# Kernel tuning notes

Measured on AMD Instinct MI355X. Metric: run time of the kernel, lower is better.

The kernel has to match this reference:

```python
import jax, jax.numpy as jnp
import numpy as np

NUM_GRAPHS = 64
NODE_SZ = 200
FEAT = 200
HID = 256          # hidden_size; each signed branch outputs HID//2
HALF = HID // 2
N_NODES = NUM_GRAPHS * NODE_SZ
N_EDGES = 409600
NUM_LAYERS = 3


def _lin_init(key, out_f, in_f):
    kw, kb = jax.random.split(key)
    s = 1.0 / np.sqrt(in_f)
    W = jax.random.uniform(kw, (out_f, in_f), minval=-s, maxval=s, dtype=jnp.float32)
    b = jax.random.uniform(kb, (out_f,), minval=-s, maxval=s, dtype=jnp.float32)
    return W, b


def setup_inputs() -> dict:
    key = jax.random.key(0)
    ks = jax.random.split(key, 16)
    x = jax.random.normal(ks[0], (N_NODES, FEAT), dtype=jnp.float32)
    edge_index = jax.random.randint(ks[1], (2, N_EDGES), 0, N_NODES, dtype=jnp.int64)
    edge_weight = jax.random.normal(ks[2], (N_EDGES,), dtype=jnp.float32)
    batch = jnp.repeat(jnp.arange(NUM_GRAPHS, dtype=jnp.int64), NODE_SZ)

    # signed conv layer params: layer0 in=FEAT, layers 1..: in=HID; each lin maps 2*in -> HALF
    Wp0, bp0 = _lin_init(ks[3], HALF, 2 * FEAT)
    Wn0, bn0 = _lin_init(ks[4], HALF, 2 * FEAT)
    Wp1, bp1 = _lin_init(ks[5], HALF, 2 * HID)
    Wn1, bn1 = _lin_init(ks[6], HALF, 2 * HID)
    Wp2, bp2 = _lin_init(ks[7], HALF, 2 * HID)
    Wn2, bn2 = _lin_init(ks[8], HALF, 2 * HID)
    Wr, br = _lin_init(ks[9], HID, NODE_SZ * HID)   # readout_lin
    Wl, bl = _lin_init(ks[10], 1, HID)              # final lin
    return dict(x=x, edge_index=edge_index, edge_weight=edge_weight, batch=batch,
                Wp0=Wp0, bp0=bp0, Wn0=Wn0, bn0=bn0,
                Wp1=Wp1, bp1=bp1, Wn1=Wn1, bn1=bn1,
                Wp2=Wp2, bp2=bp2, Wn2=Wn2, bn2=bn2,
                Wr=Wr, br=br, Wl=Wl, bl=bl)


def _signed_conv(x, src, dst, w, Wp, bp, Wn, bn):
    # edge-weighted signed mean aggregation, split by weight sign
    xs = x[src]                                   # [E, D] gather
    pw = jnp.where(w > 0, w, 0.0)
    nw = jnp.where(w < 0, -w, 0.0)
    agg_p = jax.ops.segment_sum(pw[:, None] * xs, dst, num_segments=N_NODES)
    agg_n = jax.ops.segment_sum(nw[:, None] * xs, dst, num_segments=N_NODES)
    deg_p = jax.ops.segment_sum((w > 0).astype(x.dtype), dst, num_segments=N_NODES)
    deg_n = jax.ops.segment_sum((w < 0).astype(x.dtype), dst, num_segments=N_NODES)
    agg_p = agg_p / jnp.maximum(deg_p, 1.0)[:, None]
    agg_n = agg_n / jnp.maximum(deg_n, 1.0)[:, None]
    hp = jnp.concatenate([agg_p, x], -1) @ Wp.T + bp
    hn = jnp.concatenate([agg_n, x], -1) @ Wn.T + bn
    return jnp.concatenate([hp, hn], -1)          # [N, HID]


def reference(x, edge_index, edge_weight, batch,
              Wp0, bp0, Wn0, bn0, Wp1, bp1, Wn1, bn1, Wp2, bp2, Wn2, bn2,
              Wr, br, Wl, bl):
    src, dst = edge_index[0], edge_index[1]
    convs = [(Wp0, bp0, Wn0, bn0), (Wp1, bp1, Wn1, bn1), (Wp2, bp2, Wn2, bn2)]
    h = x
    for i, (Wp, bp, Wn, bn) in enumerate(convs):
        h = _signed_conv(h, src, dst, edge_weight, Wp, bp, Wn, bn)
        if i < NUM_LAYERS - 1:
            h = jax.nn.leaky_relu(h, negative_slope=0.01)
    # per-graph readout: batch is contiguous with NODE_SZ nodes per graph,
    # so the boolean-mask+view loop is exactly a reshape.
    g = h.reshape(NUM_GRAPHS, NODE_SZ * HID)
    g = g @ Wr.T + br                             # [G, HID]
    # dropout(p=0.5) is identity in eval mode
    return g @ Wl.T + bl                          # [G, 1]
```

## Files before the change

### kernel.cpp

```cpp
#include <hip/hip_runtime.h>

#define NUM_GRAPHS 64
#define NODE_SZ    200
#define FEAT       200
#define HID        256
#define HALF       128
#define N_NODES    (NUM_GRAPHS * NODE_SZ)
#define KREAD      (NODE_SZ * HID)
#define KSTRIDE    512
#define HBLK       128

typedef unsigned short ushort_t;
typedef unsigned int uint_t;
typedef __attribute__((ext_vector_type(8))) short bf16x8;
typedef __attribute__((ext_vector_type(4))) float f32x4;

#define GAS(p) ((const __attribute__((address_space(1))) void*)(p))
#define LAS(p) ((__attribute__((address_space(3))) void*)(p))

__device__ __forceinline__ float bf2f(ushort_t u) {
    union { unsigned int i; float f; } v; v.i = ((unsigned int)u) << 16; return v.f;
}
__device__ __forceinline__ ushort_t f2bf(float f) {
    union { float f; unsigned int i; } v; v.f = f;
    unsigned int x = v.i;
    unsigned int r = (x + 0x7fffu + ((x >> 16) & 1u)) >> 16;
    return (ushort_t)r;
}

__global__ __launch_bounds__(1024) void bhist_kernel(const int* __restrict__ ei,
                                                     const float* __restrict__ ew,
                                                     uint_t* __restrict__ bh, int E) {
    __shared__ uint_t h[N_NODES];
    for (int i = threadIdx.x; i < N_NODES; i += 1024) h[i] = 0;
    __syncthreads();
    int b = blockIdx.x;
    int epb = (E + HBLK - 1) / HBLK;
    int e0 = b * epb, e1 = min(e0 + epb, E);
    for (int e = e0 + threadIdx.x; e < e1; e += 1024) {
        int dst = ei[E + e];
        float w = ew[e];
        if (w > 0.0f)      atomicAdd(&h[dst], 1u);
        else if (w < 0.0f) atomicAdd(&h[dst], 0x10000u);
    }
    __syncthreads();
    uint_t* out = bh + (size_t)b * N_NODES;
    for (int i = threadIdx.x * 4; i < N_NODES; i += 4096)
        *(uint4*)&out[i] = *(const uint4*)&h[i];
}

__global__ void colpref_kernel(uint_t* __restrict__ bh, int* __restrict__ counts,
                               int* __restrict__ cnt_p) {
    int n = blockIdx.x * 256 + threadIdx.x;
    if (n >= N_NODES) return;
    uint_t seq = 0;
#pragma unroll 1
    for (int b = 0; b < HBLK; b += 8) {
        uint_t v[8];
#pragma unroll
        for (int j = 0; j < 8; ++j) v[j] = bh[(size_t)(b + j) * N_NODES + n];
#pragma unroll
        for (int j = 0; j < 8; ++j) {
            bh[(size_t)(b + j) * N_NODES + n] = seq;
            seq += v[j];
        }
    }
    counts[n] = (int)((seq & 0xffffu) + (seq >> 16));
    cnt_p[n]  = (int)(seq & 0xffffu);
}

__global__ __launch_bounds__(1024) void scan_kernel(const int* __restrict__ counts,
                                                    const int* __restrict__ cnt_p,
                                                    uint2* __restrict__ obnd, int n) {
    const int PER = 13;
    int t = threadIdx.x;
    int start = t * PER;
    int local[PER];
    int sum = 0;
#pragma unroll
    for (int i = 0; i < PER; ++i) {
        int idx = start + i;
        int v = (idx < n) ? counts[idx] : 0;
        local[i] = sum;
        sum += v;
    }
    int lane = t & 63, wid = t >> 6;
    int inc = sum;
#pragma unroll
    for (int d = 1; d < 64; d <<= 1) {
        int up = __shfl_up(inc, d);
        if (lane >= d) inc += up;
    }
    __shared__ int wsum[16], woff[16];
    if (lane == 63) wsum[wid] = inc;
    __syncthreads();
    if (t < 16) {
        int acc = 0;
        for (int j = 0; j < 16; ++j) if (j < t) acc += wsum[j];
        woff[t] = acc;
    }
    __syncthreads();
    int base = woff[wid] + (inc - sum);
#pragma unroll
    for (int i = 0; i < PER; ++i) {
        int idx = start + i;
        if (idx < n) {
            uint_t off = (uint_t)(base + local[i]);
            obnd[idx] = make_uint2(off, off + (uint_t)cnt_p[idx]);
        }
    }
    if (t == 1023) {
        uint_t tot = (uint_t)(base + sum);
        obnd[n] = make_uint2(tot, tot);
    }
}

__global__ __launch_bounds__(1024) void scat_prep_kernel(
        const int* __restrict__ ei, const float* __restrict__ ew,
        const uint_t* __restrict__ bh, const uint2* __restrict__ obnd,
        uint2* __restrict__ es, int E,
        const float* __restrict__ W0p, const float* __restrict__ W0n,
        const float* __restrict__ W1p, const float* __restrict__ W1n,
        const float* __restrict__ W2p, const float* __restrict__ W2n,
        const float* __restrict__ x,
        ushort_t* __restrict__ wcast, ushort_t* __restrict__ xb) {
    __shared__ uint_t cur[N_NODES];
    int bx = blockIdx.x;
    if (bx < HBLK) {
        const uint_t* pref = bh + (size_t)bx * N_NODES;
        for (int i = threadIdx.x * 4; i < N_NODES; i += 4096)
            *(uint4*)&cur[i] = *(const uint4*)&pref[i];
        __syncthreads();
        int epb = (E + HBLK - 1) / HBLK;
        int e0 = bx * epb, e1 = min(e0 + epb, E);
        for (int e = e0 + threadIdx.x; e < e1; e += 1024) {
            int src = ei[e];
            int dst = ei[E + e];
            float w = ew[e];
            if (w > 0.0f) {
                uint_t old = atomicAdd(&cur[dst], 1u);
                uint_t pos = obnd[dst].x + (old & 0xffffu);
                es[pos] = make_uint2((uint_t)src, __float_as_uint(w));
            } else if (w < 0.0f) {
                uint_t old = atomicAdd(&cur[dst], 0x10000u);
                uint_t pos = obnd[dst].y + (old >> 16);
                es[pos] = make_uint2((uint_t)src, __float_as_uint(-w));
            }
        }
    } else if (bx < 512) {
        int idx = (bx - 128) * 1024 + threadIdx.x;
        int task = idx >> 16;
        int within = idx & 65535;
        const float* W = (task == 0) ? W0p : (task == 1) ? W0n : (task == 2) ? W1p
                       : (task == 3) ? W1n : (task == 4) ? W2p : W2n;
        int K2 = (task < 2) ? 400 : 512;
        int row = within >> 9;
        int col = within & (KSTRIDE - 1);
        wcast[task * 65536 + within] = (col < K2) ? f2bf(W[(size_t)row * K2 + col]) : (ushort_t)0;
    } else {
        int i = ((bx - 512) * 1024 + threadIdx.x) * 4;
        if (i < N_NODES * FEAT) {
            float4 v = *(const float4*)&x[i];
            ushort4 o;
            o.x = f2bf(v.x); o.y = f2bf(v.y); o.z = f2bf(v.z); o.w = f2bf(v.w);
            *(ushort4*)&xb[i] = o;
        }
    }
}

template <int D>
__global__ __launch_bounds__(256) void agg_kernel(
        const ushort_t* __restrict__ hb,
        const uint2* __restrict__ obnd,
        const uint2* __restrict__ es,
        ushort_t* __restrict__ Ap, ushort_t* __restrict__ An) {
    constexpr int ACT = D / 4;
    int lane = threadIdx.x & 63;
    int wv   = threadIdx.x >> 6;
    int n = blockIdx.x * 4 + wv;
    int c0 = min(lane, ACT - 1) * 4;
    uint2 ob = obnd[n];
    uint_t off = ob.x, mid = ob.y, end = obnd[n + 1].x;

    float ap[4] = {0.f, 0.f, 0.f, 0.f};
    float an[4] = {0.f, 0.f, 0.f, 0.f};

#pragma unroll 1
    for (int phase = 0; phase < 2; ++phase) {
        uint_t lo = phase ? mid : off;
        uint_t hi = phase ? end : mid;
        float* acc = phase ? an : ap;
#pragma unroll 1
        for (uint_t base = lo; base < hi; base += 64) {
            int cnt = (int)min(64u, hi - base);
            uint2 rec = es[base + (uint_t)min(lane, cnt - 1)];
            int i = 0;
#pragma unroll 1
            for (; i + 8 <= cnt; i += 8) {
                int s[8]; float w[8]; uint2 p[8];
#pragma unroll
                for (int j = 0; j < 8; ++j) {
                    s[j] = __shfl((int)rec.x, i + j);
                    w[j] = __uint_as_float((uint_t)__shfl((int)rec.y, i + j));
                }
#pragma unroll
                for (int j = 0; j < 8; ++j) p[j] = *(const uint2*)&hb[(size_t)s[j] * D + c0];
#pragma unroll
                for (int j = 0; j < 8; ++j) {
                    const ushort_t* q = (const ushort_t*)&p[j];
#pragma unroll
                    for (int c = 0; c < 4; ++c) acc[c] = fmaf(w[j], bf2f(q[c]), acc[c]);
                }
            }
#pragma unroll 1
            for (; i < cnt; ++i) {
                int s = __shfl((int)rec.x, i);
                float w = __uint_as_float((uint_t)__shfl((int)rec.y, i));
                uint2 pk = *(const uint2*)&hb[(size_t)s * D + c0];
                const ushort_t* q = (const ushort_t*)&pk;
#pragma unroll
                for (int c = 0; c < 4; ++c) acc[c] = fmaf(w, bf2f(q[c]), acc[c]);
            }
        }
    }

    size_t rb = (size_t)n * KSTRIDE;
    if (lane < ACT) {
        float dp = fmaxf((float)(mid - off), 1.0f);
        float dn = fmaxf((float)(end - mid), 1.0f);
        uint2 pk = *(const uint2*)&hb[(size_t)n * D + c0];
        const ushort_t* p = (const ushort_t*)&pk;
        ushort4 os = {p[0], p[1], p[2], p[3]};
        ushort4 op, on;
        op.x = f2bf(ap[0] / dp); op.y = f2bf(ap[1] / dp);
        op.z = f2bf(ap[2] / dp); op.w = f2bf(ap[3] / dp);
        on.x = f2bf(an[0] / dn); on.y = f2bf(an[1] / dn);
        on.z = f2bf(an[2] / dn); on.w = f2bf(an[3] / dn);
        *(ushort4*)&Ap[rb + c0] = op;
        *(ushort4*)&An[rb + c0] = on;
        *(ushort4*)&Ap[rb + D + c0] = os;
        *(ushort4*)&An[rb + D + c0] = os;
    }
    if (D == 200 && lane >= 50 && lane < 54) {
        ushort4 z = {0, 0, 0, 0};
        *(ushort4*)&Ap[rb + 400 + (lane - 50) * 4] = z;
        *(ushort4*)&An[rb + 400 + (lane - 50) * 4] = z;
    }
}

template <int KSTEPS, bool LEAKY>
__global__ __launch_bounds__(256) void conv_mfma(
        const ushort_t* __restrict__ Ap, const ushort_t* __restrict__ An,
        const ushort_t* __restrict__ Wpb, const ushort_t* __restrict__ Wnb,
        const float* __restrict__ bp, const float* __restrict__ bn,
        ushort_t* __restrict__ hout) {
    __shared__ __align__(16) ushort_t As[2][32 * 32];
    __shared__ __align__(16) ushort_t Bs[2][128 * 32];
    int mBase = blockIdx.x * 32;
    bool neg = (blockIdx.y != 0);
    const ushort_t* A    = neg ? An : Ap;
    const ushort_t* W    = neg ? Wnb : Wpb;
    const float*    bias = neg ? bn : bp;
    int tid  = threadIdx.x;
    int lane = tid & 63;
    int wv   = tid >> 6;
    int r    = lane & 15;
    int quad = lane >> 4;

    int rowA = tid >> 2, colA = (tid & 3) * 8;
    const ushort_t* gA  = A + (size_t)(mBase + (rowA & 31)) * KSTRIDE + colA;
    const ushort_t* gB0 = W + (size_t)rowA * KSTRIDE + colA;
    const ushort_t* gB1 = W + (size_t)(rowA + 64) * KSTRIDE + colA;

    f32x4 acc00 = {0.f,0.f,0.f,0.f}, acc01 = {0.f,0.f,0.f,0.f};
    f32x4 acc10 = {0.f,0.f,0.f,0.f}, acc11 = {0.f,0.f,0.f,0.f};

    if (tid < 128)
        __builtin_amdgcn_global_load_lds(GAS(gA), LAS(&As[0][wv * 512]), 16, 0, 0);
    __builtin_amdgcn_global_load_lds(GAS(gB0), LAS(&Bs[0][wv * 512]), 16, 0, 0);
    __builtin_amdgcn_global_load_lds(GAS(gB1), LAS(&Bs[0][2048 + wv * 512]), 16, 0, 0);

    for (int kt = 0; kt < KSTEPS; ++kt) {
        int cur = kt & 1;
        __syncthreads();
        if (kt + 1 < KSTEPS) {
            int kB = (kt + 1) * 32;
            if (tid < 128)
                __builtin_amdgcn_global_load_lds(GAS(gA + kB), LAS(&As[cur ^ 1][wv * 512]), 16, 0, 0);
            __builtin_amdgcn_global_load_lds(GAS(gB0 + kB), LAS(&Bs[cur ^ 1][wv * 512]), 16, 0, 0);
            __builtin_amdgcn_global_load_lds(GAS(gB1 + kB), LAS(&Bs[cur ^ 1][2048 + wv * 512]), 16, 0, 0);
        }
        bf16x8 a0 = *(const bf16x8*)&As[cur][r * 32 + quad * 8];
        bf16x8 a1 = *(const bf16x8*)&As[cur][(16 + r) * 32 + quad * 8];
        bf16x8 b0 = *(const bf16x8*)&Bs[cur][(wv * 32 + r) * 32 + quad * 8];
        bf16x8 b1 = *(const bf16x8*)&Bs[cur][(wv * 32 + 16 + r) * 32 + quad * 8];
        acc00 = __builtin_amdgcn_mfma_f32_16x16x32_bf16(a0, b0, acc00, 0, 0, 0);
        acc01 = __builtin_amdgcn_mfma_f32_16x16x32_bf16(a0, b1, acc01, 0, 0, 0);
        acc10 = __builtin_amdgcn_mfma_f32_16x16x32_bf16(a1, b0, acc10, 0, 0, 0);
        acc11 = __builtin_amdgcn_mfma_f32_16x16x32_bf16(a1, b1, acc11, 0, 0, 0);
    }
    int colOff = neg ? HALF : 0;
#pragma unroll
    for (int jn = 0; jn < 2; ++jn) {
        int cl = wv * 32 + jn * 16 + r;
        float bv = bias[cl];
        f32x4 am0 = jn ? acc01 : acc00;
        f32x4 am1 = jn ? acc11 : acc10;
#pragma unroll
        for (int reg = 0; reg < 4; ++reg) {
            int m0 = mBase + quad * 4 + reg;
            int m1 = m0 + 16;
            float v0 = am0[reg] + bv;
            float v1 = am1[reg] + bv;
            if (LEAKY) {
                v0 = (v0 > 0.0f) ? v0 : 0.01f * v0;
                v1 = (v1 > 0.0f) ? v1 : 0.01f * v1;
            }
            hout[(size_t)m0 * HID + colOff + cl] = f2bf(v0);
            hout[(size_t)m1 * HID + colOff + cl] = f2bf(v1);
        }
    }
}

__global__ __launch_bounds__(256) void readout_mfma(
        const ushort_t* __restrict__ h, const float* __restrict__ Wr,
        float* __restrict__ partial) {
    __shared__ __align__(16) ushort_t As[64 * 32];
    __shared__ __align__(16) ushort_t Bs[64 * 32];
    int nBase  = blockIdx.x * 64;
    int kStart = blockIdx.y * 800;
    int tid  = threadIdx.x;
    int lane = tid & 63;
    int wv   = tid >> 6;
    int r    = lane & 15;
    int quad = lane >> 4;

    f32x4 acc[4];
#pragma unroll
    for (int j = 0; j < 4; ++j) acc[j] = (f32x4){0.f, 0.f, 0.f, 0.f};

    for (int kt = 0; kt < 25; ++kt) {
        int kBase = kStart + kt * 32;
        int lin = tid * 8;
        int row = lin >> 5, col = lin & 31;
        *(uint4*)&As[lin] = *(const uint4*)&h[(size_t)row * KREAD + kBase + col];
        {
            const float* wp = &Wr[(size_t)(nBase + row) * KREAD + kBase + col];
            float4 f0 = *(const float4*)&wp[0];
            float4 f1 = *(const float4*)&wp[4];
            ushort4 b0, b1;
            b0.x = f2bf(f0.x); b0.y = f2bf(f0.y); b0.z = f2bf(f0.z); b0.w = f2bf(f0.w);
            b1.x = f2bf(f1.x); b1.y = f2bf(f1.y); b1.z = f2bf(f1.z); b1.w = f2bf(f1.w);
            *(ushort4*)&Bs[lin]     = b0;
            *(ushort4*)&Bs[lin + 4] = b1;
        }
        __syncthreads();
        bf16x8 a = *(const bf16x8*)&As[(wv * 16 + r) * 32 + quad * 8];
#pragma unroll
        for (int j = 0; j < 4; ++j) {
            bf16x8 b = *(const bf16x8*)&Bs[(j * 16 + r) * 32 + quad * 8];
            acc[j] = __builtin_amdgcn_mfma_f32_16x16x32_bf16(a, b, acc[j], 0, 0, 0);
        }
        __syncthreads();
    }
    float* out = partial + (size_t)blockIdx.y * (64 * HID);
#pragma unroll
    for (int j = 0; j < 4; ++j) {
        int c = nBase + j * 16 + r;
#pragma unroll
        for (int reg = 0; reg < 4; ++reg) {
            int g = wv * 16 + quad * 4 + reg;
            out[g * HID + c] = acc[j][reg];
        }
    }
}

__global__ void final_kernel(const float* __restrict__ partial, const float* __restrict__ br,
                             const float* __restrict__ Wl, const float* __restrict__ bl,
                             float* __restrict__ out) {
    int g = blockIdx.x;
    int c = threadIdx.x;
    float s = 0.0f;
#pragma unroll 4
    for (int k = 0; k < 64; ++k) s += partial[(size_t)k * (64 * HID) + g * HID + c];
    float v = (s + br[c]) * Wl[c];
#pragma unroll
    for (int d = 32; d > 0; d >>= 1) v += __shfl_down(v, d);
    __shared__ float sh[4];
    if ((c & 63) == 0) sh[c >> 6] = v;
    __syncthreads();
    if (c == 0) out[g] = sh[0] + sh[1] + sh[2] + sh[3] + bl[0];
}

extern "C" void kernel_launch(void* const* d_in, const int* in_sizes, int n_in,
                              void* d_out, int out_size, void* d_ws, size_t ws_size,
                              hipStream_t stream) {
    const float* x  = (const float*)d_in[0];
    const int*   ei = (const int*)d_in[1];
    const float* ew = (const float*)d_in[2];
    const float* Wp0 = (const float*)d_in[4];
    const float* bp0 = (const float*)d_in[5];
    const float* Wn0 = (const float*)d_in[6];
    const float* bn0 = (const float*)d_in[7];
    const float* Wp1 = (const float*)d_in[8];
    const float* bp1 = (const float*)d_in[9];
    const float* Wn1 = (const float*)d_in[10];
    const float* bn1 = (const float*)d_in[11];
    const float* Wp2 = (const float*)d_in[12];
    const float* bp2 = (const float*)d_in[13];
    const float* Wn2 = (const float*)d_in[14];
    const float* bn2 = (const float*)d_in[15];
    const float* Wr  = (const float*)d_in[16];
    const float* br  = (const float*)d_in[17];
    const float* Wl  = (const float*)d_in[18];
    const float* bl  = (const float*)d_in[19];
    const int E = in_sizes[1] / 2;

    char* ws = (char*)d_ws;
    float*    partial = (float*)(ws + 0);
    uint_t*   bh      = (uint_t*)(ws + 4194304);
    int*      counts  = (int*)(ws + 10747904);
    int*      cnt_p   = (int*)(ws + 10799104);
    uint2*    obnd    = (uint2*)(ws + 10850304);
    uint2*    es      = (uint2*)(ws + 10952768);
    ushort_t* Ap      = (ushort_t*)(ws + 14229568);
    ushort_t* An      = (ushort_t*)(ws + 27336768);
    ushort_t* hA      = (ushort_t*)(ws + 40443968);
    ushort_t* hB      = (ushort_t*)(ws + 46997568);
    ushort_t* wcast   = (ushort_t*)(ws + 53551168);
    ushort_t* xb      = (ushort_t*)(ws + 54337600);

    ushort_t* w0p = wcast + 0 * 65536;
    ushort_t* w0n = wcast + 1 * 65536;
    ushort_t* w1p = wcast + 2 * 65536;
    ushort_t* w1n = wcast + 3 * 65536;
    ushort_t* w2p = wcast + 4 * 65536;
    ushort_t* w2n = wcast + 5 * 65536;

    hipLaunchKernelGGL(bhist_kernel, dim3(HBLK), dim3(1024), 0, stream, ei, ew, bh, E);
    hipLaunchKernelGGL(colpref_kernel, dim3((N_NODES + 255) / 256), dim3(256), 0, stream,
                       bh, counts, cnt_p);
    hipLaunchKernelGGL(scan_kernel, dim3(1), dim3(1024), 0, stream, counts, cnt_p, obnd, N_NODES);
    hipLaunchKernelGGL(scat_prep_kernel, dim3(1137), dim3(1024), 0, stream,
                       ei, ew, bh, obnd, es, E,
                       Wp0, Wn0, Wp1, Wn1, Wp2, Wn2, x, wcast, xb);

    hipLaunchKernelGGL((agg_kernel<FEAT>), dim3(N_NODES / 4), dim3(256), 0, stream,
                       xb, obnd, es, Ap, An);
    hipLaunchKernelGGL((conv_mfma<13, true>), dim3(N_NODES / 32, 2), dim3(256), 0, stream,
                       Ap, An, w0p, w0n, bp0, bn0, hA);
    hipLaunchKernelGGL((agg_kernel<HID>), dim3(N_NODES / 4), dim3(256), 0, stream,
                       hA, obnd, es, Ap, An);
    hipLaunchKernelGGL((conv_mfma<16, true>), dim3(N_NODES / 32, 2), dim3(256), 0, stream,
                       Ap, An, w1p, w1n, bp1, bn1, hB);
    hipLaunchKernelGGL((agg_kernel<HID>), dim3(N_NODES / 4), dim3(256), 0, stream,
                       hB, obnd, es, Ap, An);
    hipLaunchKernelGGL((conv_mfma<16, false>), dim3(N_NODES / 32, 2), dim3(256), 0, stream,
                       Ap, An, w2p, w2n, bp2, bn2, hA);

    hipLaunchKernelGGL(readout_mfma, dim3(4, 64), dim3(256), 0, stream, hA, Wr, partial);
    hipLaunchKernelGGL(final_kernel, dim3(NUM_GRAPHS), dim3(256), 0, stream,
                       partial, br, Wl, bl, (float*)d_out);
}
```

Baseline: 310.4 us.

## Transform node features before aggregation instead of aggregating then transforming

Reorders each signed conv layer by linearity: a single GEMM first projects each node's features through the concatenated weight blocks (W_agg_p, W_agg_n, W_self_p, W_self_n) into a 512-wide Y. A combine kernel then gathers only the 128-wide projected rows per edge, scales by the inverse degree and adds the self term, bias and LeakyReLU. The gather moves 128 bf16 values per edge instead of 200 or 256, and the wide concatenated Ap/An buffers disappear. In exchange the GEMM output is twice as wide, and the aggregation now sums bf16-rounded projections, which changes rounding.

```diff
diff --git a/kernel.cpp b/kernel.cpp
--- a/kernel.cpp
+++ b/kernel.cpp
@@ -7,7 +7,6 @@
 #define HALF       128
 #define N_NODES    (NUM_GRAPHS * NODE_SZ)
 #define KREAD      (NODE_SZ * HID)
-#define KSTRIDE    512
 #define HBLK       128
 
 typedef unsigned short ushort_t;
@@ -123,7 +122,7 @@
         const float* __restrict__ W1p, const float* __restrict__ W1n,
         const float* __restrict__ W2p, const float* __restrict__ W2n,
         const float* __restrict__ x,
-        ushort_t* __restrict__ wcast, ushort_t* __restrict__ xb) {
+        ushort_t* __restrict__ wall, ushort_t* __restrict__ xb) {
     __shared__ uint_t cur[N_NODES];
     int bx = blockIdx.x;
     if (bx < HBLK) {
@@ -149,118 +148,41 @@
         }
     } else if (bx < 512) {
         int idx = (bx - 128) * 1024 + threadIdx.x;
-        int task = idx >> 16;
-        int within = idx & 65535;
-        const float* W = (task == 0) ? W0p : (task == 1) ? W0n : (task == 2) ? W1p
-                       : (task == 3) ? W1n : (task == 4) ? W2p : W2n;
-        int K2 = (task < 2) ? 400 : 512;
-        int row = within >> 9;
-        int col = within & (KSTRIDE - 1);
-        wcast[task * 65536 + within] = (col < K2) ? f2bf(W[(size_t)row * K2 + col]) : (ushort_t)0;
+        int layer = idx >> 17;
+        int within = idx & 131071;
+        int rr = within >> 8;
+        int col = within & 255;
+        const float* Wp = (layer == 0) ? W0p : (layer == 1) ? W1p : W2p;
+        const float* Wn = (layer == 0) ? W0n : (layer == 1) ? W1n : W2n;
+        int Ks = (layer == 0) ? 200 : 256;
+        int q = rr >> 7;
+        const float* Wsrc = (q & 1) ? Wn : Wp;
+        int row = rr & 127;
+        int scol = col + ((q >> 1) ? Ks : 0);
+        float v = (col < Ks) ? Wsrc[(size_t)row * (2 * Ks) + scol] : 0.0f;
+        wall[idx] = f2bf(v);
     } else {
-        int i = ((bx - 512) * 1024 + threadIdx.x) * 4;
-        if (i < N_NODES * FEAT) {
-            float4 v = *(const float4*)&x[i];
-            ushort4 o;
+        int idx = (bx - 512) * 1024 + threadIdx.x;
+        int n = idx >> 6;
+        int c0 = (idx & 63) * 4;
+        ushort4 o = {0, 0, 0, 0};
+        if (c0 < 200) {
+            float4 v = *(const float4*)&x[(size_t)n * 200 + c0];
             o.x = f2bf(v.x); o.y = f2bf(v.y); o.z = f2bf(v.z); o.w = f2bf(v.w);
-            *(ushort4*)&xb[i] = o;
-        }
-    }
-}
-
-template <int D>
-__global__ __launch_bounds__(256) void agg_kernel(
-        const ushort_t* __restrict__ hb,
-        const uint2* __restrict__ obnd,
-        const uint2* __restrict__ es,
-        ushort_t* __restrict__ Ap, ushort_t* __restrict__ An) {
-    constexpr int ACT = D / 4;
-    int lane = threadIdx.x & 63;
-    int wv   = threadIdx.x >> 6;
-    int n = blockIdx.x * 4 + wv;
-    int c0 = min(lane, ACT - 1) * 4;
-    uint2 ob = obnd[n];
-    uint_t off = ob.x, mid = ob.y, end = obnd[n + 1].x;
-
-    float ap[4] = {0.f, 0.f, 0.f, 0.f};
-    float an[4] = {0.f, 0.f, 0.f, 0.f};
-
-#pragma unroll 1
-    for (int phase = 0; phase < 2; ++phase) {
-        uint_t lo = phase ? mid : off;
-        uint_t hi = phase ? end : mid;
-        float* acc = phase ? an : ap;
-#pragma unroll 1
-        for (uint_t base = lo; base < hi; base += 64) {
-            int cnt = (int)min(64u, hi - base);
-            uint2 rec = es[base + (uint_t)min(lane, cnt - 1)];
-            int i = 0;
-#pragma unroll 1
-            for (; i + 8 <= cnt; i += 8) {
-                int s[8]; float w[8]; uint2 p[8];
-#pragma unroll
-                for (int j = 0; j < 8; ++j) {
-                    s[j] = __shfl((int)rec.x, i + j);
-                    w[j] = __uint_as_float((uint_t)__shfl((int)rec.y, i + j));
-                }
-#pragma unroll
-                for (int j = 0; j < 8; ++j) p[j] = *(const uint2*)&hb[(size_t)s[j] * D + c0];
-#pragma unroll
-                for (int j = 0; j < 8; ++j) {
-                    const ushort_t* q = (const ushort_t*)&p[j];
-#pragma unroll
-                    for (int c = 0; c < 4; ++c) acc[c] = fmaf(w[j], bf2f(q[c]), acc[c]);
-                }
-            }
-#pragma unroll 1
-            for (; i < cnt; ++i) {
-                int s = __shfl((int)rec.x, i);
-                float w = __uint_as_float((uint_t)__shfl((int)rec.y, i));
-                uint2 pk = *(const uint2*)&hb[(size_t)s * D + c0];
-                const ushort_t* q = (const ushort_t*)&pk;
-#pragma unroll
-                for (int c = 0; c < 4; ++c) acc[c] = fmaf(w, bf2f(q[c]), acc[c]);
-            }
-        }
-    }
-
-    size_t rb = (size_t)n * KSTRIDE;
-    if (lane < ACT) {
-        float dp = fmaxf((float)(mid - off), 1.0f);
-        float dn = fmaxf((float)(end - mid), 1.0f);
-        uint2 pk = *(const uint2*)&hb[(size_t)n * D + c0];
-        const ushort_t* p = (const ushort_t*)&pk;
-        ushort4 os = {p[0], p[1], p[2], p[3]};
-        ushort4 op, on;
-        op.x = f2bf(ap[0] / dp); op.y = f2bf(ap[1] / dp);
-        op.z = f2bf(ap[2] / dp); op.w = f2bf(ap[3] / dp);
-        on.x = f2bf(an[0] / dn); on.y = f2bf(an[1] / dn);
-        on.z = f2bf(an[2] / dn); on.w = f2bf(an[3] / dn);
-        *(ushort4*)&Ap[rb + c0] = op;
-        *(ushort4*)&An[rb + c0] = on;
-        *(ushort4*)&Ap[rb + D + c0] = os;
-        *(ushort4*)&An[rb + D + c0] = os;
-    }
-    if (D == 200 && lane >= 50 && lane < 54) {
-        ushort4 z = {0, 0, 0, 0};
-        *(ushort4*)&Ap[rb + 400 + (lane - 50) * 4] = z;
-        *(ushort4*)&An[rb + 400 + (lane - 50) * 4] = z;
-    }
-}
-
-template <int KSTEPS, bool LEAKY>
-__global__ __launch_bounds__(256) void conv_mfma(
-        const ushort_t* __restrict__ Ap, const ushort_t* __restrict__ An,
-        const ushort_t* __restrict__ Wpb, const ushort_t* __restrict__ Wnb,
-        const float* __restrict__ bp, const float* __restrict__ bn,
-        ushort_t* __restrict__ hout) {
+        }
+        *(ushort4*)&xb[(size_t)n * 256 + c0] = o;
+    }
+}
+
+template <int KSTEPS>
+__global__ __launch_bounds__(256) void gemm_mfma(
+        const ushort_t* __restrict__ A,
+        const ushort_t* __restrict__ B,
+        ushort_t* __restrict__ Y) {
     __shared__ __align__(16) ushort_t As[2][32 * 32];
     __shared__ __align__(16) ushort_t Bs[2][128 * 32];
     int mBase = blockIdx.x * 32;
-    bool neg = (blockIdx.y != 0);
-    const ushort_t* A    = neg ? An : Ap;
-    const ushort_t* W    = neg ? Wnb : Wpb;
-    const float*    bias = neg ? bn : bp;
+    int nBase = blockIdx.y * 128;
     int tid  = threadIdx.x;
     int lane = tid & 63;
     int wv   = tid >> 6;
@@ -268,9 +190,9 @@
     int quad = lane >> 4;
 
     int rowA = tid >> 2, colA = (tid & 3) * 8;
-    const ushort_t* gA  = A + (size_t)(mBase + (rowA & 31)) * KSTRIDE + colA;
-    const ushort_t* gB0 = W + (size_t)rowA * KSTRIDE + colA;
-    const ushort_t* gB1 = W + (size_t)(rowA + 64) * KSTRIDE + colA;
+    const ushort_t* gA  = A + (size_t)(mBase + (rowA & 31)) * 256 + colA;
+    const ushort_t* gB0 = B + (size_t)(nBase + rowA) * 256 + colA;
+    const ushort_t* gB1 = B + (size_t)(nBase + rowA + 64) * 256 + colA;
 
     f32x4 acc00 = {0.f,0.f,0.f,0.f}, acc01 = {0.f,0.f,0.f,0.f};
     f32x4 acc10 = {0.f,0.f,0.f,0.f}, acc11 = {0.f,0.f,0.f,0.f};
@@ -299,27 +221,94 @@
         acc10 = __builtin_amdgcn_mfma_f32_16x16x32_bf16(a1, b0, acc10, 0, 0, 0);
         acc11 = __builtin_amdgcn_mfma_f32_16x16x32_bf16(a1, b1, acc11, 0, 0, 0);
     }
-    int colOff = neg ? HALF : 0;
 #pragma unroll
     for (int jn = 0; jn < 2; ++jn) {
-        int cl = wv * 32 + jn * 16 + r;
-        float bv = bias[cl];
+        int cl = nBase + wv * 32 + jn * 16 + r;
         f32x4 am0 = jn ? acc01 : acc00;
         f32x4 am1 = jn ? acc11 : acc10;
 #pragma unroll
         for (int reg = 0; reg < 4; ++reg) {
             int m0 = mBase + quad * 4 + reg;
-            int m1 = m0 + 16;
-            float v0 = am0[reg] + bv;
-            float v1 = am1[reg] + bv;
-            if (LEAKY) {
-                v0 = (v0 > 0.0f) ? v0 : 0.01f * v0;
-                v1 = (v1 > 0.0f) ? v1 : 0.01f * v1;
+            Y[(size_t)m0 * 512 + cl]        = f2bf(am0[reg]);
+            Y[(size_t)(m0 + 16) * 512 + cl] = f2bf(am1[reg]);
+        }
+    }
+}
+
+template <bool LEAKY>
+__global__ __launch_bounds__(256) void aggcomb_kernel(
+        const ushort_t* __restrict__ Y,
+        const uint2* __restrict__ obnd,
+        const uint2* __restrict__ es,
+        const float* __restrict__ bp, const float* __restrict__ bn,
+        ushort_t* __restrict__ out) {
+    int lane = threadIdx.x & 63;
+    int wv   = threadIdx.x >> 6;
+    int n = blockIdx.x * 4 + wv;
+    int c0 = lane * 2;
+    uint2 ob = obnd[n];
+    uint_t off = ob.x, mid = ob.y, end = obnd[n + 1].x;
+
+    float accp[2] = {0.f, 0.f};
+    float accn[2] = {0.f, 0.f};
+
+#pragma unroll 1
+    for (int phase = 0; phase < 2; ++phase) {
+        uint_t lo = phase ? mid : off;
+        uint_t hi = phase ? end : mid;
+        float* acc = phase ? accn : accp;
+        const ushort_t* Yb = Y + (phase ? 128 : 0) + c0;
+#pragma unroll 1
+        for (uint_t base = lo; base < hi; base += 64) {
+            int cnt = (int)min(64u, hi - base);
+            uint2 rec = es[base + (uint_t)min(lane, cnt - 1)];
+            int i = 0;
+#pragma unroll 1
+            for (; i + 8 <= cnt; i += 8) {
+                int s[8]; float w[8]; uint_t u[8];
+#pragma unroll
+                for (int j = 0; j < 8; ++j) {
+                    s[j] = __shfl((int)rec.x, i + j);
+                    w[j] = __uint_as_float((uint_t)__shfl((int)rec.y, i + j));
+                }
+#pragma unroll
+                for (int j = 0; j < 8; ++j) u[j] = *(const uint_t*)&Yb[(size_t)s[j] * 512];
+#pragma unroll
+                for (int j = 0; j < 8; ++j) {
+                    acc[0] = fmaf(w[j], bf2f((ushort_t)(u[j] & 0xffffu)), acc[0]);
+                    acc[1] = fmaf(w[j], bf2f((ushort_t)(u[j] >> 16)), acc[1]);
+                }
             }
-            hout[(size_t)m0 * HID + colOff + cl] = f2bf(v0);
-            hout[(size_t)m1 * HID + colOff + cl] = f2bf(v1);
-        }
-    }
+#pragma unroll 1
+            for (; i < cnt; ++i) {
+                int s = __shfl((int)rec.x, i);
+                float w = __uint_as_float((uint_t)__shfl((int)rec.y, i));
+                uint_t u = *(const uint_t*)&Yb[(size_t)s * 512];
+                acc[0] = fmaf(w, bf2f((ushort_t)(u & 0xffffu)), acc[0]);
+                acc[1] = fmaf(w, bf2f((ushort_t)(u >> 16)), acc[1]);
+            }
+        }
+    }
+
+    float dp = fmaxf((float)(mid - off), 1.0f);
+    float dn = fmaxf((float)(end - mid), 1.0f);
+    float rp = 1.0f / dp, rn = 1.0f / dn;
+    uint_t zp = *(const uint_t*)&Y[(size_t)n * 512 + 256 + c0];
+    uint_t zn = *(const uint_t*)&Y[(size_t)n * 512 + 384 + c0];
+    float vp0 = fmaf(accp[0], rp, bf2f((ushort_t)(zp & 0xffffu)) + bp[c0]);
+    float vp1 = fmaf(accp[1], rp, bf2f((ushort_t)(zp >> 16))     + bp[c0 + 1]);
+    float vn0 = fmaf(accn[0], rn, bf2f((ushort_t)(zn & 0xffffu)) + bn[c0]);
+    float vn1 = fmaf(accn[1], rn, bf2f((ushort_t)(zn >> 16))     + bn[c0 + 1]);
+    if (LEAKY) {
+        vp0 = (vp0 > 0.0f) ? vp0 : 0.01f * vp0;
+        vp1 = (vp1 > 0.0f) ? vp1 : 0.01f * vp1;
+        vn0 = (vn0 > 0.0f) ? vn0 : 0.01f * vn0;
+        vn1 = (vn1 > 0.0f) ? vn1 : 0.01f * vn1;
+    }
+    uint_t op = (uint_t)f2bf(vp0) | ((uint_t)f2bf(vp1) << 16);
+    uint_t on = (uint_t)f2bf(vn0) | ((uint_t)f2bf(vn1) << 16);
+    *(uint_t*)&out[(size_t)n * 256 + c0]       = op;
+    *(uint_t*)&out[(size_t)n * 256 + 128 + c0] = on;
 }
 
 __global__ __launch_bounds__(256) void readout_mfma(
@@ -423,40 +412,32 @@
     int*      cnt_p   = (int*)(ws + 10799104);
     uint2*    obnd    = (uint2*)(ws + 10850304);
     uint2*    es      = (uint2*)(ws + 10952768);
-    ushort_t* Ap      = (ushort_t*)(ws + 14229568);
-    ushort_t* An      = (ushort_t*)(ws + 27336768);
-    ushort_t* hA      = (ushort_t*)(ws + 40443968);
-    ushort_t* hB      = (ushort_t*)(ws + 46997568);
-    ushort_t* wcast   = (ushort_t*)(ws + 53551168);
-    ushort_t* xb      = (ushort_t*)(ws + 54337600);
-
-    ushort_t* w0p = wcast + 0 * 65536;
-    ushort_t* w0n = wcast + 1 * 65536;
-    ushort_t* w1p = wcast + 2 * 65536;
-    ushort_t* w1n = wcast + 3 * 65536;
-    ushort_t* w2p = wcast + 4 * 65536;
-    ushort_t* w2n = wcast + 5 * 65536;
+    ushort_t* Yall    = (ushort_t*)(ws + 14229568);
+    ushort_t* hA      = (ushort_t*)(ws + 27336768);
+    ushort_t* hB      = (ushort_t*)(ws + 33890368);
+    ushort_t* wall    = (ushort_t*)(ws + 40443968);
+    ushort_t* xb      = (ushort_t*)(ws + 41230400);
 
     hipLaunchKernelGGL(bhist_kernel, dim3(HBLK), dim3(1024), 0, stream, ei, ew, bh, E);
     hipLaunchKernelGGL(colpref_kernel, dim3((N_NODES + 255) / 256), dim3(256), 0, stream,
                        bh, counts, cnt_p);
     hipLaunchKernelGGL(scan_kernel, dim3(1), dim3(1024), 0, stream, counts, cnt_p, obnd, N_NODES);
-    hipLaunchKernelGGL(scat_prep_kernel, dim3(1137), dim3(1024), 0, stream,
+    hipLaunchKernelGGL(scat_prep_kernel, dim3(1312), dim3(1024), 0, stream,
                        ei, ew, bh, obnd, es, E,
-                       Wp0, Wn0, Wp1, Wn1, Wp2, Wn2, x, wcast, xb);
-
-    hipLaunchKernelGGL((agg_kernel<FEAT>), dim3(N_NODES / 4), dim3(256), 0, stream,
-                       xb, obnd, es, Ap, An);
-    hipLaunchKernelGGL((conv_mfma<13, true>), dim3(N_NODES / 32, 2), dim3(256), 0, stream,
-                       Ap, An, w0p, w0n, bp0, bn0, hA);
-    hipLaunchKernelGGL((agg_kernel<HID>), dim3(N_NODES / 4), dim3(256), 0, stream,
-                       hA, obnd, es, Ap, An);
-    hipLaunchKernelGGL((conv_mfma<16, true>), dim3(N_NODES / 32, 2), dim3(256), 0, stream,
-                       Ap, An, w1p, w1n, bp1, bn1, hB);
-    hipLaunchKernelGGL((agg_kernel<HID>), dim3(N_NODES / 4), dim3(256), 0, stream,
-                       hB, obnd, es, Ap, An);
-    hipLaunchKernelGGL((conv_mfma<16, false>), dim3(N_NODES / 32, 2), dim3(256), 0, stream,
-                       Ap, An, w2p, w2n, bp2, bn2, hA);
+                       Wp0, Wn0, Wp1, Wn1, Wp2, Wn2, x, wall, xb);
+
+    hipLaunchKernelGGL((gemm_mfma<7>), dim3(N_NODES / 32, 4), dim3(256), 0, stream,
+                       xb, wall + 0 * 131072, Yall);
+    hipLaunchKernelGGL((aggcomb_kernel<true>), dim3(N_NODES / 4), dim3(256), 0, stream,
+                       Yall, obnd, es, bp0, bn0, hA);
+    hipLaunchKernelGGL((gemm_mfma<8>), dim3(N_NODES / 32, 4), dim3(256), 0, stream,
+                       hA, wall + 1 * 131072, Yall);
+    hipLaunchKernelGGL((aggcomb_kernel<true>), dim3(N_NODES / 4), dim3(256), 0, stream,
+                       Yall, obnd, es, bp1, bn1, hB);
+    hipLaunchKernelGGL((gemm_mfma<8>), dim3(N_NODES / 32, 4), dim3(256), 0, stream,
+                       hB, wall + 2 * 131072, Yall);
+    hipLaunchKernelGGL((aggcomb_kernel<false>), dim3(N_NODES / 4), dim3(256), 0, stream,
+                       Yall, obnd, es, bp2, bn2, hA);
 
     hipLaunchKernelGGL(readout_mfma, dim3(4, 64), dim3(256), 0, stream, hA, Wr, partial);
     hipLaunchKernelGGL(final_kernel, dim3(NUM_GRAPHS), dim3(256), 0, stream,
```

Result: faster. 296.8 us (-4.4%).
